# Optimization experiments

Measured on AMD Instinct MI355X. Metric: run time of the kernel, lower is better.

## Reference

```python
import jax, jax.numpy as jnp
import numpy as np

GROUP = 32
HEADS = 8
EPS = 1e-5


def setup_inputs() -> dict:
    key = jax.random.key(0)
    k1, k2, k3 = jax.random.split(key, 3)
    C = 512
    x = jax.random.normal(k1, (8, C, 32, 32), dtype=jnp.float32)
    gn_w = jnp.ones((C,), dtype=jnp.float32)
    gn_b = jnp.zeros((C,), dtype=jnp.float32)
    # 1x1 convs == channel matmuls; init like torch conv default (kaiming-ish scale)
    w_qkv = jax.random.normal(k2, (3 * C, C), dtype=jnp.float32) * (1.0 / np.sqrt(C))
    w_proj = jax.random.normal(k3, (C, C), dtype=jnp.float32) * (1.0 / np.sqrt(C))
    return {"x": x, "gn_w": gn_w, "gn_b": gn_b, "w_qkv": w_qkv, "w_proj": w_proj}


def _forward(x, gn_w, gn_b, w_qkv, w_proj):
    B, C, H, W = x.shape
    N = H * W
    d = C // HEADS
    scale = d ** -0.5
    # GroupNorm over (channels_per_group, H, W)
    xg = x.reshape(B, GROUP, C // GROUP, H, W)
    mean = xg.mean(axis=(2, 3, 4), keepdims=True)
    var = xg.var(axis=(2, 3, 4), keepdims=True)
    xn = ((xg - mean) * jax.lax.rsqrt(var + EPS)).reshape(B, C, H, W)
    xn = xn * gn_w[None, :, None, None] + gn_b[None, :, None, None]
    # 1x1 conv QKV: [3C, C] x [B, C, H, W]
    qkv = jnp.einsum('oc,bchw->bohw', w_qkv, xn)
    q, k, v = jnp.split(qkv, 3, axis=1)

    def to_heads(t):  # b (h d) H W -> b h N d
        return t.reshape(B, HEADS, d, N).transpose(0, 1, 3, 2)

    q, k, v = to_heads(q), to_heads(k), to_heads(v)
    scores = jnp.einsum('bhid,bhjd->bhij', q, k) * scale
    probs = jax.nn.softmax(scores, axis=-1)
    out = jnp.einsum('bhij,bhjd->bhid', probs, v)
    # b h N d -> b (h d) H W
    out = out.transpose(0, 1, 3, 2).reshape(B, C, H, W)
    out = jnp.einsum('oc,bchw->bohw', w_proj, out)
    return x + out


def reference(x, gn_w, gn_b, w_qkv, w_proj):
    return _forward(x, gn_w, gn_b, w_qkv, w_proj)
```

## Files before the change

### kernel.cpp

```cpp
#include <hip/hip_runtime.h>

typedef __attribute__((ext_vector_type(4))) float f32x4;
typedef __attribute__((ext_vector_type(8))) __bf16 bf16x8;
typedef __attribute__((ext_vector_type(8))) unsigned short ushort8;

#define BATCH 8
#define CH    512
#define NN    1024
#define GRP   32
#define NHEAD 8
#define DH    64
#define QBLK  128
#define KBLK  64

static constexpr size_t OFF_STATS = 0;
static constexpr size_t OFF_WQB   = 4096;
static constexpr size_t OFF_WPB   = OFF_WQB + (size_t)1536*512*2;
static constexpr size_t OFF_XNT   = OFF_WPB + (size_t)512*512*2;
static constexpr size_t OFF_QKB   = OFF_XNT + (size_t)BATCH*NN*CH*2;
static constexpr size_t OFF_VT    = OFF_QKB + (size_t)BATCH*NN*1024*2;
static constexpr size_t OFF_ATTNT = OFF_VT  + (size_t)BATCH*CH*NN*2;

static __device__ __forceinline__ unsigned short f2bf(float f){
  union { float f; unsigned u; } cv; cv.f = f;
  unsigned u = cv.u;
  u += 0x7fffu + ((u >> 16) & 1u);
  return (unsigned short)(u >> 16);
}

static __device__ __forceinline__ void gload_lds16(const unsigned short* g, unsigned short* l){
  __builtin_amdgcn_global_load_lds((const __attribute__((address_space(1))) void*)g,
                                   (__attribute__((address_space(3))) void*)l, 16, 0, 0);
}

__global__ __launch_bounds__(256) void cvt_w_k(const float* __restrict__ wq, const float* __restrict__ wp,
                                               unsigned short* __restrict__ wqb, unsigned short* __restrict__ wpb){
  int i = blockIdx.x*256 + threadIdx.x;
  if (i < 1536*512) wqb[i] = f2bf(wq[i]);
  if (i < 512*512)  wpb[i] = f2bf(wp[i]);
}

__global__ __launch_bounds__(256) void gn_stats_k(const float* __restrict__ x, float* __restrict__ stats){
  int bg = blockIdx.x;
  const float4* base = (const float4*)(x + (size_t)bg * (16*NN));
  float s = 0.f, ss = 0.f;
  #pragma unroll 4
  for (int idx = threadIdx.x; idx < 16*NN/4; idx += 256){
    float4 v = base[idx];
    s  += (v.x + v.y) + (v.z + v.w);
    ss += (v.x*v.x + v.y*v.y) + (v.z*v.z + v.w*v.w);
  }
  for (int off = 32; off > 0; off >>= 1){ s += __shfl_down(s, off); ss += __shfl_down(ss, off); }
  __shared__ float red[8];
  int w = threadIdx.x >> 6, l = threadIdx.x & 63;
  if (l == 0){ red[w*2] = s; red[w*2+1] = ss; }
  __syncthreads();
  if (threadIdx.x == 0){
    float S  = red[0]+red[2]+red[4]+red[6];
    float SS = red[1]+red[3]+red[5]+red[7];
    float mean = S * (1.f/(16*NN));
    float var  = SS * (1.f/(16*NN)) - mean*mean;
    stats[bg*2]   = mean;
    stats[bg*2+1] = rsqrtf(var + 1e-5f);
  }
}

__global__ __launch_bounds__(256) void gn_apply_k(const float* __restrict__ x, const float* __restrict__ stats,
                                                  const float* __restrict__ gw, const float* __restrict__ gb,
                                                  unsigned short* __restrict__ xnT){
  int b = blockIdx.z, c0 = blockIdx.y*64, n0 = blockIdx.x*64;
  __shared__ unsigned short T[64][65];
  int t = threadIdx.x;
  int nl = t & 63;
  int cb = t >> 6;
  #pragma unroll
  for (int r = 0; r < 16; ++r){
    int cl = cb + r*4;
    int c  = c0 + cl;
    float xv   = x[((size_t)b*CH + c)*NN + n0 + nl];
    float mean = stats[(b*GRP + (c>>4))*2];
    float rstd = stats[(b*GRP + (c>>4))*2 + 1];
    float sc   = rstd * gw[c];
    T[cl][nl]  = f2bf((xv - mean)*sc + gb[c]);
  }
  __syncthreads();
  #pragma unroll
  for (int r = 0; r < 16; ++r){
    int nlocal = cb + r*4;
    xnT[((size_t)b*NN + n0 + nlocal)*CH + c0 + nl] = T[nl][nlocal];
  }
}

__global__ __launch_bounds__(256) void qkv_gemm_k(const unsigned short* __restrict__ wq,
                                                  const unsigned short* __restrict__ xnT,
                                                  unsigned short* __restrict__ qkb,
                                                  unsigned short* __restrict__ vT){
  int b  = blockIdx.z;
  int m0 = blockIdx.y * 128;
  int n0 = blockIdx.x * 128;
  __shared__ unsigned short As[128][64];
  __shared__ unsigned short Bs[128][64];
  int t = threadIdx.x;
  int w = t >> 6, l = t & 63;
  int wm = w >> 1, wn = w & 1;
  f32x4 acc[4][4] = {};
  const unsigned short* Ag = wq  + (size_t)(m0 + w*32)*512;
  const unsigned short* Bg = xnT + ((size_t)b*NN + n0 + w*32)*512;
  int r8 = l >> 3;
  int c8 = ((l & 7) ^ r8) * 8;
  int lr = l & 15, lg = l >> 4;
  int xr = (lr & 7) << 3;
  for (int k0 = 0; k0 < 512; k0 += 64){
    #pragma unroll
    for (int i = 0; i < 4; ++i){
      gload_lds16(Ag + (size_t)(i*8 + r8)*512 + k0 + c8, &As[w*32 + i*8][0]);
      gload_lds16(Bg + (size_t)(i*8 + r8)*512 + k0 + c8, &Bs[w*32 + i*8][0]);
    }
    __syncthreads();
    #pragma unroll
    for (int ks = 0; ks < 2; ++ks){
      bf16x8 af[4], bfr[4];
      #pragma unroll
      for (int mf = 0; mf < 4; ++mf) af[mf]  = *(const bf16x8*)&As[wm*64 + mf*16 + lr][(ks*32 + lg*8) ^ xr];
      #pragma unroll
      for (int nf = 0; nf < 4; ++nf) bfr[nf] = *(const bf16x8*)&Bs[wn*64 + nf*16 + lr][(ks*32 + lg*8) ^ xr];
      #pragma unroll
      for (int mf = 0; mf < 4; ++mf)
        #pragma unroll
        for (int nf = 0; nf < 4; ++nf)
          acc[mf][nf] = __builtin_amdgcn_mfma_f32_16x16x32_bf16(af[mf], bfr[nf], acc[mf][nf], 0, 0, 0);
    }
    __syncthreads();
  }
  int lq = l >> 4;
  float scl = (m0 < 512) ? 0.18033688f : 1.0f;
  if (m0 < 1024){
    #pragma unroll
    for (int mf = 0; mf < 4; ++mf)
      #pragma unroll
      for (int nf = 0; nf < 4; ++nf)
        #pragma unroll
        for (int r = 0; r < 4; ++r){
          int o = m0 + wm*64 + mf*16 + lq*4 + r;
          int n = n0 + wn*64 + nf*16 + lr;
          qkb[((size_t)b*NN + n)*1024 + o] = f2bf(acc[mf][nf][r] * scl);
        }
  } else {
    #pragma unroll
    for (int mf = 0; mf < 4; ++mf)
      #pragma unroll
      for (int nf = 0; nf < 4; ++nf)
        #pragma unroll
        for (int r = 0; r < 4; ++r){
          int o = m0 + wm*64 + mf*16 + lq*4 + r;
          int n = n0 + wn*64 + nf*16 + lr;
          vT[((size_t)b*512 + (o - 1024))*NN + n] = f2bf(acc[mf][nf][r]);
        }
  }
}

#define ATTN_TILE(CUR, NXT, J0, PF)                                                         \
  {                                                                                          \
    f32x4 s[2][4] = {};                                                                      \
    _Pragma("unroll") for (int ks = 0; ks < 2; ++ks)                                         \
      _Pragma("unroll") for (int mf = 0; mf < 2; ++mf)                                       \
        _Pragma("unroll") for (int nf = 0; nf < 4; ++nf)                                     \
          s[mf][nf] = __builtin_amdgcn_mfma_f32_16x16x32_bf16(qf[mf][ks], CUR[ks][nf], s[mf][nf], 0, 0, 0); \
    if (PF) {                                                                                \
      _Pragma("unroll") for (int ks = 0; ks < 2; ++ks)                                       \
        _Pragma("unroll") for (int nf = 0; nf < 4; ++nf)                                     \
          NXT[ks][nf] = *(const bf16x8*)(Kbase + (size_t)((J0) + KBLK + nf*16 + lr)*1024 + ks*32 + lg*8); \
    }                                                                                        \
    bf16x8 vf[2][4];                                                                         \
    _Pragma("unroll") for (int ks = 0; ks < 2; ++ks)                                         \
      _Pragma("unroll") for (int nf = 0; nf < 4; ++nf)                                       \
        vf[ks][nf] = *(const bf16x8*)(Vbase + (size_t)(nf*16 + lr)*NN + (J0) + ks*32 + lg*8);\
    _Pragma("unroll") for (int mf = 0; mf < 2; ++mf)                                         \
      _Pragma("unroll") for (int nf = 0; nf < 4; ++nf)                                       \
        _Pragma("unroll") for (int r = 0; r < 4; ++r){                                       \
          float p = exp2f(s[mf][nf][r]);                                                     \
          lsum[mf][r] += p;                                                                  \
          Ps[w][mf*16 + lg*4 + r][nf*16 + lr] = (__bf16)p;                                   \
        }                                                                                    \
    asm volatile("s_waitcnt lgkmcnt(0)" ::: "memory");                                       \
    __builtin_amdgcn_sched_barrier(0);                                                       \
    _Pragma("unroll") for (int ks = 0; ks < 2; ++ks){                                        \
      bf16x8 pf[2];                                                                          \
      _Pragma("unroll") for (int mf = 0; mf < 2; ++mf)                                       \
        pf[mf] = *(const bf16x8*)&Ps[w][mf*16 + lr][ks*32 + lg*8];                           \
      _Pragma("unroll") for (int mf = 0; mf < 2; ++mf)                                       \
        _Pragma("unroll") for (int nf = 0; nf < 4; ++nf)                                     \
          acc_o[mf][nf] = __builtin_amdgcn_mfma_f32_16x16x32_bf16(pf[mf], vf[ks][nf], acc_o[mf][nf], 0, 0, 0); \
    }                                                                                        \
  }

__global__ __launch_bounds__(256) void attn_k(const unsigned short* __restrict__ qkb,
                                              const unsigned short* __restrict__ vT,
                                              unsigned short* __restrict__ attnT){
  int bh = blockIdx.x;
  int b = bh >> 3, h = bh & 7;
  int q0 = blockIdx.y * QBLK;
  int t = threadIdx.x;
  int w = t >> 6, l = t & 63;
  int lr = l & 15, lg = l >> 4;

  __shared__ __bf16 Ps[4][32][72];

  bf16x8 qf[2][2];
  #pragma unroll
  for (int mf = 0; mf < 2; ++mf)
    #pragma unroll
    for (int ks = 0; ks < 2; ++ks){
      int row = q0 + w*32 + mf*16 + lr;
      qf[mf][ks] = *(const bf16x8*)(qkb + ((size_t)b*NN + row)*1024 + h*DH + ks*32 + lg*8);
    }

  float lsum[2][4] = {};
  f32x4 acc_o[2][4] = {};

  const unsigned short* Kbase = qkb + (size_t)b*NN*1024 + 512 + h*DH;
  const unsigned short* Vbase = vT  + (size_t)(b*NHEAD + h)*DH*NN;

  bf16x8 kfA[2][4], kfB[2][4];
  #pragma unroll
  for (int ks = 0; ks < 2; ++ks)
    #pragma unroll
    for (int nf = 0; nf < 4; ++nf)
      kfA[ks][nf] = *(const bf16x8*)(Kbase + (size_t)(nf*16 + lr)*1024 + ks*32 + lg*8);

  for (int j0 = 0; j0 < NN; j0 += 2*KBLK){
    ATTN_TILE(kfA, kfB, j0, true)
    ATTN_TILE(kfB, kfA, (j0 + KBLK), (j0 + 2*KBLK < NN))
  }

  #pragma unroll
  for (int st = 1; st < 16; st <<= 1)
    #pragma unroll
    for (int mf = 0; mf < 2; ++mf)
      #pragma unroll
      for (int r = 0; r < 4; ++r)
        lsum[mf][r] += __shfl_xor(lsum[mf][r], st);

  #pragma unroll
  for (int mf = 0; mf < 2; ++mf)
    #pragma unroll
    for (int r = 0; r < 4; ++r) lsum[mf][r] = 1.f / lsum[mf][r];

  #pragma unroll
  for (int mf = 0; mf < 2; ++mf)
    #pragma unroll
    for (int nf = 0; nf < 4; ++nf)
      #pragma unroll
      for (int r = 0; r < 4; ++r){
        int row = q0 + w*32 + mf*16 + lg*4 + r;
        int col = h*DH + nf*16 + lr;
        attnT[((size_t)b*NN + row)*CH + col] = f2bf(acc_o[mf][nf][r] * lsum[mf][r]);
      }
}

__global__ __launch_bounds__(256) void proj_gemm_k(const unsigned short* __restrict__ wp,
                                                   const unsigned short* __restrict__ attnT,
                                                   const float* __restrict__ x, float* __restrict__ out){
  int b  = blockIdx.z;
  int m0 = blockIdx.y * 64;
  int n0 = blockIdx.x * 128;
  __shared__ unsigned short As[64][64];
  __shared__ unsigned short Bs[128][64];
  int t = threadIdx.x;
  int w = t >> 6, l = t & 63;
  int wm = w >> 1, wn = w & 1;
  f32x4 acc[2][4] = {};
  const unsigned short* Ag = wp    + (size_t)(m0 + w*16)*512;
  const unsigned short* Bg = attnT + ((size_t)b*NN + n0 + w*32)*512;
  int r8 = l >> 3;
  int c8 = ((l & 7) ^ r8) * 8;
  int lr = l & 15, lg = l >> 4;
  int xr = (lr & 7) << 3;
  for (int k0 = 0; k0 < 512; k0 += 64){
    #pragma unroll
    for (int i = 0; i < 2; ++i)
      gload_lds16(Ag + (size_t)(i*8 + r8)*512 + k0 + c8, &As[w*16 + i*8][0]);
    #pragma unroll
    for (int i = 0; i < 4; ++i)
      gload_lds16(Bg + (size_t)(i*8 + r8)*512 + k0 + c8, &Bs[w*32 + i*8][0]);
    __syncthreads();
    #pragma unroll
    for (int ks = 0; ks < 2; ++ks){
      bf16x8 af[2], bfr[4];
      #pragma unroll
      for (int mf = 0; mf < 2; ++mf) af[mf]  = *(const bf16x8*)&As[wm*32 + mf*16 + lr][(ks*32 + lg*8) ^ xr];
      #pragma unroll
      for (int nf = 0; nf < 4; ++nf) bfr[nf] = *(const bf16x8*)&Bs[wn*64 + nf*16 + lr][(ks*32 + lg*8) ^ xr];
      #pragma unroll
      for (int mf = 0; mf < 2; ++mf)
        #pragma unroll
        for (int nf = 0; nf < 4; ++nf)
          acc[mf][nf] = __builtin_amdgcn_mfma_f32_16x16x32_bf16(af[mf], bfr[nf], acc[mf][nf], 0, 0, 0);
    }
    __syncthreads();
  }
  int lq = l >> 4;
  #pragma unroll
  for (int mf = 0; mf < 2; ++mf)
    #pragma unroll
    for (int nf = 0; nf < 4; ++nf)
      #pragma unroll
      for (int r = 0; r < 4; ++r){
        int o = m0 + wm*32 + mf*16 + lq*4 + r;
        int n = n0 + wn*64 + nf*16 + lr;
        size_t idx = ((size_t)b*CH + o)*NN + n;
        out[idx] = x[idx] + acc[mf][nf][r];
      }
}

extern "C" void kernel_launch(void* const* d_in, const int* in_sizes, int n_in,
                              void* d_out, int out_size, void* d_ws, size_t ws_size,
                              hipStream_t stream){
  const float* x  = (const float*)d_in[0];
  const float* gw = (const float*)d_in[1];
  const float* gb = (const float*)d_in[2];
  const float* wq = (const float*)d_in[3];
  const float* wp = (const float*)d_in[4];
  float* out = (float*)d_out;
  char* ws = (char*)d_ws;
  float*          stats = (float*)(ws + OFF_STATS);
  unsigned short* wqb   = (unsigned short*)(ws + OFF_WQB);
  unsigned short* wpb   = (unsigned short*)(ws + OFF_WPB);
  unsigned short* xnT   = (unsigned short*)(ws + OFF_XNT);
  unsigned short* qkb   = (unsigned short*)(ws + OFF_QKB);
  unsigned short* vT    = (unsigned short*)(ws + OFF_VT);
  unsigned short* attnT = (unsigned short*)(ws + OFF_ATTNT);

  hipLaunchKernelGGL(cvt_w_k,    dim3(3072),      dim3(256), 0, stream, wq, wp, wqb, wpb);
  hipLaunchKernelGGL(gn_stats_k, dim3(256),       dim3(256), 0, stream, x, stats);
  hipLaunchKernelGGL(gn_apply_k, dim3(16, 8, 8),  dim3(256), 0, stream, x, stats, gw, gb, xnT);
  hipLaunchKernelGGL(qkv_gemm_k, dim3(8, 12, 8),  dim3(256), 0, stream, wqb, xnT, qkb, vT);
  hipLaunchKernelGGL(attn_k,     dim3(64, 8),     dim3(256), 0, stream, qkb, vT, attnT);
  hipLaunchKernelGGL(proj_gemm_k,dim3(8, 8, 8),   dim3(256), 0, stream, wpb, attnT, x, out);
}
```

Baseline: 175.0 us.

## Stage K/V tiles in LDS with async loads and compute transposed scores

Rewrites the attention kernel so K and V tiles are copied into double-buffered, XOR-swizzled LDS with global_load_lds and shared by all four waves, instead of each wave loading them from global memory into registers. Scores are computed transposed (K as the A operand), so the P tile can be rearranged with cross-lane shuffles rather than a round trip through an LDS scratch buffer. MFMA sections are wrapped in s_setprio, and the output is staged through LDS to allow 16-byte coalesced stores. It adds a block-wide barrier per KV tile and relies on exact layout and shuffle index arithmetic for correctness.

After: 155.7 us. 1.12x faster.

```diff
diff --git a/kernel.cpp b/kernel.cpp
--- a/kernel.cpp
+++ b/kernel.cpp
@@ -26,6 +26,12 @@
   unsigned u = cv.u;
   u += 0x7fffu + ((u >> 16) & 1u);
   return (unsigned short)(u >> 16);
+}
+
+static __device__ __forceinline__ unsigned pack2bf(float lo, float hi){
+  union { __bf16 h[2]; unsigned u; } v;
+  v.h[0] = (__bf16)lo; v.h[1] = (__bf16)hi;
+  return v.u;
 }
 
 static __device__ __forceinline__ void gload_lds16(const unsigned short* g, unsigned short* l){
@@ -159,39 +165,15 @@
   }
 }
 
-#define ATTN_TILE(CUR, NXT, J0, PF)                                                         \
-  {                                                                                          \
-    f32x4 s[2][4] = {};                                                                      \
-    _Pragma("unroll") for (int ks = 0; ks < 2; ++ks)                                         \
-      _Pragma("unroll") for (int mf = 0; mf < 2; ++mf)                                       \
-        _Pragma("unroll") for (int nf = 0; nf < 4; ++nf)                                     \
-          s[mf][nf] = __builtin_amdgcn_mfma_f32_16x16x32_bf16(qf[mf][ks], CUR[ks][nf], s[mf][nf], 0, 0, 0); \
-    if (PF) {                                                                                \
-      _Pragma("unroll") for (int ks = 0; ks < 2; ++ks)                                       \
-        _Pragma("unroll") for (int nf = 0; nf < 4; ++nf)                                     \
-          NXT[ks][nf] = *(const bf16x8*)(Kbase + (size_t)((J0) + KBLK + nf*16 + lr)*1024 + ks*32 + lg*8); \
-    }                                                                                        \
-    bf16x8 vf[2][4];                                                                         \
-    _Pragma("unroll") for (int ks = 0; ks < 2; ++ks)                                         \
-      _Pragma("unroll") for (int nf = 0; nf < 4; ++nf)                                       \
-        vf[ks][nf] = *(const bf16x8*)(Vbase + (size_t)(nf*16 + lr)*NN + (J0) + ks*32 + lg*8);\
-    _Pragma("unroll") for (int mf = 0; mf < 2; ++mf)                                         \
-      _Pragma("unroll") for (int nf = 0; nf < 4; ++nf)                                       \
-        _Pragma("unroll") for (int r = 0; r < 4; ++r){                                       \
-          float p = exp2f(s[mf][nf][r]);                                                     \
-          lsum[mf][r] += p;                                                                  \
-          Ps[w][mf*16 + lg*4 + r][nf*16 + lr] = (__bf16)p;                                   \
-        }                                                                                    \
-    asm volatile("s_waitcnt lgkmcnt(0)" ::: "memory");                                       \
-    __builtin_amdgcn_sched_barrier(0);                                                       \
-    _Pragma("unroll") for (int ks = 0; ks < 2; ++ks){                                        \
-      bf16x8 pf[2];                                                                          \
-      _Pragma("unroll") for (int mf = 0; mf < 2; ++mf)                                       \
-        pf[mf] = *(const bf16x8*)&Ps[w][mf*16 + lr][ks*32 + lg*8];                           \
-      _Pragma("unroll") for (int mf = 0; mf < 2; ++mf)                                       \
-        _Pragma("unroll") for (int nf = 0; nf < 4; ++nf)                                     \
-          acc_o[mf][nf] = __builtin_amdgcn_mfma_f32_16x16x32_bf16(pf[mf], vf[ks][nf], acc_o[mf][nf], 0, 0, 0); \
-    }                                                                                        \
+#define STAGE_KV(TT, BUF)                                                                \
+  {                                                                                      \
+    int jj = (TT) * KBLK;                                                                \
+    _Pragma("unroll") for (int ch = 0; ch < 2; ++ch){                                    \
+      gload_lds16(Kg + (size_t)(jj + w*16 + ch*8 + srow)*1024 + scol,                    \
+                  &KV[0][BUF][w*16 + ch*8][0]);                                          \
+      gload_lds16(Vg + (size_t)(w*16 + ch*8 + srow)*NN + jj + scol,                      \
+                  &KV[1][BUF][w*16 + ch*8][0]);                                          \
+    }                                                                                    \
   }
 
 __global__ __launch_bounds__(256) void attn_k(const unsigned short* __restrict__ qkb,
@@ -204,7 +186,12 @@
   int w = t >> 6, l = t & 63;
   int lr = l & 15, lg = l >> 4;
 
-  __shared__ __bf16 Ps[4][32][72];
+  __shared__ unsigned short KV[2][2][64][64];
+
+  int srow = l >> 3;
+  int scol = ((l & 7) ^ srow) * 8;
+  const unsigned short* Kg = qkb + (size_t)b*NN*1024 + 512 + h*DH;
+  const unsigned short* Vg = vT  + (size_t)(b*NHEAD + h)*DH*NN;
 
   bf16x8 qf[2][2];
   #pragma unroll
@@ -215,47 +202,98 @@
       qf[mf][ks] = *(const bf16x8*)(qkb + ((size_t)b*NN + row)*1024 + h*DH + ks*32 + lg*8);
     }
 
-  float lsum[2][4] = {};
-  f32x4 acc_o[2][4] = {};
-
-  const unsigned short* Kbase = qkb + (size_t)b*NN*1024 + 512 + h*DH;
-  const unsigned short* Vbase = vT  + (size_t)(b*NHEAD + h)*DH*NN;
-
-  bf16x8 kfA[2][4], kfB[2][4];
-  #pragma unroll
-  for (int ks = 0; ks < 2; ++ks)
+  float lsum[2] = {0.f, 0.f};
+  f32x4 accO[2][4] = {};
+
+  STAGE_KV(0, 0)
+  __syncthreads();
+
+  for (int tt = 0; tt < 16; ++tt){
+    int cur = tt & 1;
+    if (tt < 15) STAGE_KV(tt + 1, cur ^ 1)
+    int xr = (lr & 7) * 8;
+    bf16x8 kf[2][4], vf[2][4];
+    #pragma unroll
+    for (int ks = 0; ks < 2; ++ks)
+      #pragma unroll
+      for (int nf = 0; nf < 4; ++nf){
+        kf[ks][nf] = *(const bf16x8*)&KV[0][cur][nf*16 + lr][(ks*32 + lg*8) ^ xr];
+        vf[ks][nf] = *(const bf16x8*)&KV[1][cur][nf*16 + lr][(ks*32 + lg*8) ^ xr];
+      }
+    #pragma unroll
+    for (int mf = 0; mf < 2; ++mf){
+      f32x4 sT[4] = {};
+      __builtin_amdgcn_s_setprio(1);
+      #pragma unroll
+      for (int ks = 0; ks < 2; ++ks)
+        #pragma unroll
+        for (int nf = 0; nf < 4; ++nf)
+          sT[nf] = __builtin_amdgcn_mfma_f32_16x16x32_bf16(kf[ks][nf], qf[mf][ks], sT[nf], 0, 0, 0);
+      __builtin_amdgcn_s_setprio(0);
+      unsigned pk[4][2];
+      #pragma unroll
+      for (int nf = 0; nf < 4; ++nf){
+        float p0 = exp2f(sT[nf][0]), p1 = exp2f(sT[nf][1]);
+        float p2 = exp2f(sT[nf][2]), p3 = exp2f(sT[nf][3]);
+        lsum[mf] += (p0 + p1) + (p2 + p3);
+        pk[nf][0] = pack2bf(p0, p1);
+        pk[nf][1] = pack2bf(p2, p3);
+      }
+      int srcA = lr + ((lg & 1) << 5);
+      int srcB = srcA + 16;
+      bool hsel = (lg >> 1) != 0;
+      #pragma unroll
+      for (int ks = 0; ks < 2; ++ks){
+        unsigned a0 = (unsigned)__shfl((int)pk[2*ks  ][0], srcA);
+        unsigned a1 = (unsigned)__shfl((int)pk[2*ks  ][1], srcA);
+        unsigned a2 = (unsigned)__shfl((int)pk[2*ks  ][0], srcB);
+        unsigned a3 = (unsigned)__shfl((int)pk[2*ks  ][1], srcB);
+        unsigned b0 = (unsigned)__shfl((int)pk[2*ks+1][0], srcA);
+        unsigned b1 = (unsigned)__shfl((int)pk[2*ks+1][1], srcA);
+        unsigned b2 = (unsigned)__shfl((int)pk[2*ks+1][0], srcB);
+        unsigned b3 = (unsigned)__shfl((int)pk[2*ks+1][1], srcB);
+        union { unsigned u[4]; bf16x8 v; } pf;
+        pf.u[0] = hsel ? b0 : a0;
+        pf.u[1] = hsel ? b1 : a1;
+        pf.u[2] = hsel ? b2 : a2;
+        pf.u[3] = hsel ? b3 : a3;
+        __builtin_amdgcn_s_setprio(1);
+        #pragma unroll
+        for (int nf = 0; nf < 4; ++nf)
+          accO[mf][nf] = __builtin_amdgcn_mfma_f32_16x16x32_bf16(vf[ks][nf], pf.v, accO[mf][nf], 0, 0, 0);
+        __builtin_amdgcn_s_setprio(0);
+      }
+    }
+    __syncthreads();
+  }
+
+  #pragma unroll
+  for (int mf = 0; mf < 2; ++mf){
+    lsum[mf] += __shfl_xor(lsum[mf], 16);
+    lsum[mf] += __shfl_xor(lsum[mf], 32);
+    lsum[mf] = 1.f / lsum[mf];
+  }
+
+  unsigned short* Ob = &KV[0][0][0][0] + w * 2304;
+  #pragma unroll
+  for (int mf = 0; mf < 2; ++mf)
     #pragma unroll
     for (int nf = 0; nf < 4; ++nf)
-      kfA[ks][nf] = *(const bf16x8*)(Kbase + (size_t)(nf*16 + lr)*1024 + ks*32 + lg*8);
-
-  for (int j0 = 0; j0 < NN; j0 += 2*KBLK){
-    ATTN_TILE(kfA, kfB, j0, true)
-    ATTN_TILE(kfB, kfA, (j0 + KBLK), (j0 + 2*KBLK < NN))
-  }
-
-  #pragma unroll
-  for (int st = 1; st < 16; st <<= 1)
-    #pragma unroll
-    for (int mf = 0; mf < 2; ++mf)
-      #pragma unroll
-      for (int r = 0; r < 4; ++r)
-        lsum[mf][r] += __shfl_xor(lsum[mf][r], st);
-
-  #pragma unroll
-  for (int mf = 0; mf < 2; ++mf)
-    #pragma unroll
-    for (int r = 0; r < 4; ++r) lsum[mf][r] = 1.f / lsum[mf][r];
-
-  #pragma unroll
-  for (int mf = 0; mf < 2; ++mf)
-    #pragma unroll
-    for (int nf = 0; nf < 4; ++nf)
       #pragma unroll
       for (int r = 0; r < 4; ++r){
-        int row = q0 + w*32 + mf*16 + lg*4 + r;
-        int col = h*DH + nf*16 + lr;
-        attnT[((size_t)b*NN + row)*CH + col] = f2bf(acc_o[mf][nf][r] * lsum[mf][r]);
-      }
+        __bf16 hv = (__bf16)(accO[mf][nf][r] * lsum[mf]);
+        Ob[mf*1152 + lr*72 + nf*16 + lg*4 + r] = *(unsigned short*)&hv;
+      }
+  __syncthreads();
+  int qr = l >> 2, cc = (l & 3) * 16;
+  #pragma unroll
+  for (int mf = 0; mf < 2; ++mf){
+    bf16x8 o0 = *(const bf16x8*)&Ob[mf*1152 + qr*72 + cc];
+    bf16x8 o1 = *(const bf16x8*)&Ob[mf*1152 + qr*72 + cc + 8];
+    unsigned short* dst = attnT + ((size_t)b*NN + q0 + w*32 + mf*16 + qr)*CH + h*DH + cc;
+    *(bf16x8*)dst = o0;
+    *(bf16x8*)(dst + 8) = o1;
+  }
 }
 
 __global__ __launch_bounds__(256) void proj_gemm_k(const unsigned short* __restrict__ wp,
```
